# Kernel tuning notes

Measured on AMD Instinct MI355X. Metric: run time of the kernel, lower is better.

The kernel has to match this reference:

```python
import jax, jax.numpy as jnp
import numpy as np

B, S, D, H = 2, 2048, 1024, 16
DK = D // H


def setup_inputs() -> dict:
    key = jax.random.key(0)
    ks = jax.random.split(key, 8)
    Q = jax.random.normal(ks[0], (B, S, D), dtype=jnp.float32)
    K = jax.random.normal(ks[1], (B, S, D), dtype=jnp.float32)
    V = jax.random.normal(ks[2], (B, S, D), dtype=jnp.float32)
    # causal mask (1 = keep), broadcastable to [B, H, S, S]
    mask = jnp.tril(jnp.ones((S, S), dtype=bool))[None, None, :, :]
    # xavier_uniform for [D, D]: bound = sqrt(6 / (D + D))
    bound = float(np.sqrt(6.0 / (D + D)))
    def xavier(k):
        return jax.random.uniform(k, (D, D), jnp.float32, -bound, bound)
    Wq, Wk, Wv, Wo = xavier(ks[3]), xavier(ks[4]), xavier(ks[5]), xavier(ks[6])
    bq = jnp.zeros((D,), jnp.float32)
    bk = jnp.zeros((D,), jnp.float32)
    bv = jnp.zeros((D,), jnp.float32)
    bo = jnp.zeros((D,), jnp.float32)
    return {"Q": Q, "K": K, "V": V, "mask": mask,
            "Wq": Wq, "bq": bq, "Wk": Wk, "bk": bk,
            "Wv": Wv, "bv": bv, "Wo": Wo, "bo": bo}


def _split_heads(x):
    # [B, S, D] -> [B, H, S, DK]
    b, s, _ = x.shape
    return x.reshape(b, s, H, DK).transpose(0, 2, 1, 3)


def reference(Q, K, V, mask, Wq, bq, Wk, bk, Wv, bv, Wo, bo):
    # linear projections (torch Linear: x @ W.T + b)
    q = _split_heads(Q @ Wq.T + bq)  # [B, H, S, DK]
    k = _split_heads(K @ Wk.T + bk)
    v = _split_heads(V @ Wv.T + bv)
    scale = 1.0 / jnp.sqrt(jnp.asarray(DK, q.dtype))
    scores = jnp.einsum('bhqd,bhkd->bhqk', q, k) * scale  # [B, H, S, S]
    scores = jnp.where(mask, scores, jnp.asarray(-1e9, scores.dtype))
    attn = jax.nn.softmax(scores, axis=-1)
    ctx = jnp.einsum('bhqk,bhkd->bhqd', attn, v)  # [B, H, S, DK]
    ctx = ctx.transpose(0, 2, 1, 3).reshape(Q.shape[0], Q.shape[1], D)
    out = ctx @ Wo.T + bo  # dropout is identity in eval mode
    return out, attn
```

## Files before the change

### kernel.cpp

```cpp
#include <hip/hip_runtime.h>
#include <hip/hip_bf16.h>

#define B_  2
#define S_  2048
#define D_  1024
#define H_  16
#define DK_ 64
#define M_  (B_*S_)
#define NT_ (S_/64)
#define NE_ (B_*S_*D_)
#define NW_ (D_*D_)

typedef __attribute__((ext_vector_type(8))) short short8;
typedef __attribute__((ext_vector_type(4))) float f32x4;

static __device__ __forceinline__ unsigned short f2bf(float f) {
    union { float f; unsigned u; } v; v.f = f;
    unsigned r = (v.u + 0x7fffu + ((v.u >> 16) & 1u)) >> 16;
    return (unsigned short)r;
}

static __device__ __forceinline__ void gload16(const void* g, void* l) {
    __builtin_amdgcn_global_load_lds((const __attribute__((address_space(1))) void*)g,
                                     (__attribute__((address_space(3))) void*)l, 16, 0, 0);
}

__global__ __launch_bounds__(256) void conv7(const float* __restrict__ q,  const float* __restrict__ k,
                                             const float* __restrict__ v,  const float* __restrict__ wq,
                                             const float* __restrict__ wk, const float* __restrict__ wv,
                                             const float* __restrict__ wo, unsigned short* __restrict__ ws)
{
    const float* src[7] = {q, k, v, wq, wk, wv, wo};
    const int    n4[7]  = {NE_/4, NE_/4, NE_/4, NW_/4, NW_/4, NW_/4, NW_/4};
    size_t off = 0;
    #pragma unroll
    for (int seg = 0; seg < 7; ++seg) {
        unsigned short* dst = ws + off;
        for (int i = blockIdx.x*256 + threadIdx.x; i < n4[seg]; i += gridDim.x*256) {
            float4 x = ((const float4*)src[seg])[i];
            union { unsigned short u[4]; unsigned long long ll; } cv;
            cv.u[0]=f2bf(x.x); cv.u[1]=f2bf(x.y); cv.u[2]=f2bf(x.z); cv.u[3]=f2bf(x.w);
            ((unsigned long long*)dst)[i] = cv.ll;
        }
        off += (size_t)n4[seg]*4;
    }
}

__global__ __launch_bounds__(256) void gemm_bt(const unsigned short* __restrict__ A0,
                                               const unsigned short* __restrict__ W0,
                                               const float* __restrict__ b0,
                                               const float* __restrict__ b1,
                                               const float* __restrict__ b2,
                                               void* __restrict__ outv, int out_mode)
{
    __shared__ unsigned short as2[2][128][64];
    __shared__ unsigned short bs2[2][64][64];

    const int tid  = threadIdx.x;
    const int wave = tid >> 6;
    const int lane = tid & 63;
    const int lq   = lane & 15, quad = lane >> 4;
    const int z    = blockIdx.z;
    const int m0   = blockIdx.y * 128, n0 = blockIdx.x * 64;
    const int wm   = (wave >> 1) * 64, wn = (wave & 1) * 32;

    const unsigned short* A  = A0 + (size_t)z * NE_;
    const unsigned short* Bt = W0 + (size_t)z * NW_;
    const float* bias = (z == 0) ? b0 : (z == 1 ? b1 : b2);

    f32x4 acc[4][2] = {};

    auto STAGE = [&](int k0, int buf) {
        #pragma unroll
        for (int i = 0; i < 4; ++i) {
            const int p = tid + i*256, row = p >> 3, c = (p & 7) ^ (row & 7);
            gload16(A + (size_t)(m0+row)*D_ + k0 + c*8,
                    (char*)&as2[buf][0][0] + (size_t)(wave*64 + i*256)*16);
        }
        #pragma unroll
        for (int i = 0; i < 2; ++i) {
            const int p = tid + i*256, row = p >> 3, c = (p & 7) ^ (row & 7);
            gload16(Bt + (size_t)(n0+row)*D_ + k0 + c*8,
                    (char*)&bs2[buf][0][0] + (size_t)(wave*64 + i*256)*16);
        }
    };

    STAGE(0, 0);
    __syncthreads();
    int cur = 0;
    for (int k0 = 0; k0 < D_; k0 += 64) {
        if (k0 + 64 < D_) STAGE(k0 + 64, cur ^ 1);
        #pragma unroll
        for (int kk = 0; kk < 2; ++kk) {
            short8 a[4], b[2];
            #pragma unroll
            for (int i = 0; i < 4; ++i) {
                const int row = wm + i*16 + lq;
                a[i] = *(const short8*)((const char*)&as2[cur][0][0] + row*128 + (((kk*4+quad) ^ (row&7))*16));
            }
            #pragma unroll
            for (int j = 0; j < 2; ++j) {
                const int row = wn + j*16 + lq;
                b[j] = *(const short8*)((const char*)&bs2[cur][0][0] + row*128 + (((kk*4+quad) ^ (row&7))*16));
            }
            #pragma unroll
            for (int i = 0; i < 4; ++i)
                #pragma unroll
                for (int j = 0; j < 2; ++j)
                    acc[i][j] = __builtin_amdgcn_mfma_f32_16x16x32_bf16(a[i], b[j], acc[i][j], 0, 0, 0);
        }
        __syncthreads();
        cur ^= 1;
    }

    float bcol[2];
    #pragma unroll
    for (int j = 0; j < 2; ++j) bcol[j] = bias[n0 + wn + j*16 + lq];

    if (out_mode == 0) {
        float* out = (float*)outv;
        #pragma unroll
        for (int i = 0; i < 4; ++i)
            #pragma unroll
            for (int j = 0; j < 2; ++j) {
                const int col = n0 + wn + j*16 + lq;
                #pragma unroll
                for (int r = 0; r < 4; ++r) {
                    const int m = m0 + wm + i*16 + quad*4 + r;
                    out[(size_t)m*D_ + col] = acc[i][j][r] + bcol[j];
                }
            }
    } else {
        unsigned short* out = (unsigned short*)outv + (size_t)z * NE_;
        #pragma unroll
        for (int i = 0; i < 4; ++i)
            #pragma unroll
            for (int j = 0; j < 2; ++j) {
                const int col = n0 + wn + j*16 + lq;
                const int h = col >> 6, dk = col & 63;
                #pragma unroll
                for (int r = 0; r < 4; ++r) {
                    const int m  = m0 + wm + i*16 + quad*4 + r;
                    const int bb = m >> 11, s = m & (S_-1);
                    out[(((size_t)(bb*H_ + h))*S_ + s)*DK_ + dk] = f2bf(acc[i][j][r] + bcol[j]);
                }
            }
    }
}

__global__ __launch_bounds__(256) void transpose_v(const unsigned short* __restrict__ vp,
                                                   unsigned short* __restrict__ vt)
{
    __shared__ unsigned short ts[64][72];
    const int tid = threadIdx.x;
    const int s0  = blockIdx.x * 64;
    const size_t bh = (size_t)blockIdx.z * H_ + blockIdx.y;
    const unsigned short* src = vp + (bh * S_ + s0) * DK_;
    #pragma unroll
    for (int i = 0; i < 2; ++i) {
        int idx = tid + i*256;
        *(short8*)&ts[idx >> 3][(idx & 7)*8] = *(const short8*)(src + idx*8);
    }
    __syncthreads();
    unsigned short* dst = vt + bh * DK_ * S_;
    #pragma unroll
    for (int i = 0; i < 2; ++i) {
        int idx = tid + i*256;
        int dk = idx >> 3, c = idx & 7;
        union { unsigned short u[8]; short8 v; } pk;
        #pragma unroll
        for (int j = 0; j < 8; ++j) pk.u[j] = ts[c*8 + j][dk];
        *(short8*)(dst + (size_t)dk*S_ + s0 + c*8) = pk.v;
    }
}

__global__ __launch_bounds__(512) void attn_mfma(const unsigned short* __restrict__ q,
                                                 const unsigned short* __restrict__ k,
                                                 const unsigned short* __restrict__ vt,
                                                 float* __restrict__ attn,
                                                 unsigned short* __restrict__ ctx)
{
    __shared__ unsigned short qs_es[9216];
    __shared__ unsigned short ks2[2][64][64];
    __shared__ unsigned short vts2[2][64][64];

    const int tid  = threadIdx.x;
    const int wave = tid >> 6, lane = tid & 63;
    const int lq   = lane & 15, quad = lane >> 4;
    const int ts   = wave >> 2;
    const int wr0  = (wave & 3) * 16;

    const int g = blockIdx.x;
    const int xcd = g & 7, i5 = g >> 3;
    const int x = i5 >> 2;
    const int bhid = xcd + 8*(i5 & 3);
    const int h = bhid & (H_-1), b = bhid >> 4;

    const int itA = x, itB = NT_-1 - x;
    const int itM = ts ? itB : itA;
    const size_t bh = (size_t)(b*H_ + h);
    const unsigned short* kb  = k  + bh*S_*DK_;
    const unsigned short* vtb = vt + bh*(size_t)DK_*S_;
    const unsigned short* qbA = q + (bh*S_ + (size_t)itA*64) * DK_;
    const unsigned short* qbB = q + (bh*S_ + (size_t)itB*64) * DK_;
    float* attn_bM = attn + bh*(size_t)S_*S_ + (size_t)itM*64*S_;

    {
        const int row = tid >> 3, c = (tid & 7) ^ (row & 7);
        gload16(qbA + (size_t)row*DK_ + c*8, (char*)qs_es + tid*16);
        gload16(qbB + (size_t)row*DK_ + c*8, (char*)qs_es + 8192 + tid*16);
        gload16(kb  + (size_t)row*DK_ + c*8, (char*)&ks2[0][0][0] + tid*16);
    }
    __syncthreads();

    short8 aT0, aT1;
    {
        const int row = wr0 + lq;
        const char* qrow = (const char*)qs_es + ts*8192 + row*128;
        aT0 = *(const short8*)(qrow + ((quad     ^ (row & 7)) * 16));
        aT1 = *(const short8*)(qrow + (((4+quad) ^ (row & 7)) * 16));
    }
    const int rg0 = itM*64 + wr0 + quad*4;

    float rs[4] = {0.f, 0.f, 0.f, 0.f};
    int cur = 0;
    for (int jt = 0; jt <= itB; ++jt) {
        if (jt < itB) {
            const int row = tid >> 3, c = (tid & 7) ^ (row & 7);
            gload16(kb + ((size_t)(jt+1)*64 + row)*DK_ + c*8,
                    (char*)&ks2[cur^1][0][0] + tid*16);
        }
        if (jt <= itM) {
            f32x4 sa[4];
            __builtin_amdgcn_s_setprio(1);
            #pragma unroll
            for (int j = 0; j < 4; ++j) {
                const int krow = j*16 + lq;
                const char* kp8 = (const char*)&ks2[cur][0][0] + krow*128;
                const short8 b0 = *(const short8*)(kp8 + ((quad     ^ (krow&7)) * 16));
                const short8 b1 = *(const short8*)(kp8 + (((4+quad) ^ (krow&7)) * 16));
                f32x4 s = {};
                s = __builtin_amdgcn_mfma_f32_16x16x32_bf16(aT0, b0, s, 0, 0, 0);
                s = __builtin_amdgcn_mfma_f32_16x16x32_bf16(aT1, b1, s, 0, 0, 0);
                sa[j] = s;
            }
            __builtin_amdgcn_s_setprio(0);
            #pragma unroll
            for (int j = 0; j < 4; ++j) {
                const int cg = jt*64 + j*16 + lq;
                #pragma unroll
                for (int r = 0; r < 4; ++r)
                    if (cg <= rg0 + r) rs[r] += __expf(sa[j][r]*0.125f);
            }
        }
        __syncthreads();
        cur ^= 1;
    }

    {
        const int row = tid >> 3, c = (tid & 7) ^ (row & 7);
        gload16(kb  + (size_t)row*DK_ + c*8, (char*)&ks2[0][0][0]  + tid*16);
        gload16(vtb + (size_t)row*S_  + c*8, (char*)&vts2[0][0][0] + tid*16);
    }
    #pragma unroll
    for (int m = 1; m < 16; m <<= 1)
        #pragma unroll
        for (int r = 0; r < 4; ++r) rs[r] += __shfl_xor(rs[r], m, 64);
    float inv[4];
    #pragma unroll
    for (int r = 0; r < 4; ++r) inv[r] = 1.0f / rs[r];
    __syncthreads();

    unsigned short* es = qs_es;
    f32x4 cacc[4] = {};
    cur = 0;
    for (int jt = 0; jt <= itB; ++jt) {
        if (jt < itB) {
            const int row = tid >> 3, c = (tid & 7) ^ (row & 7);
            gload16(kb  + ((size_t)(jt+1)*64 + row)*DK_ + c*8,
                    (char*)&ks2[cur^1][0][0]  + tid*16);
            gload16(vtb + (size_t)row*S_ + (jt+1)*64 + c*8,
                    (char*)&vts2[cur^1][0][0] + tid*16);
        }
        if (jt <= itM) {
            f32x4 sa[4];
            __builtin_amdgcn_s_setprio(1);
            #pragma unroll
            for (int j = 0; j < 4; ++j) {
                const int krow = j*16 + lq;
                const char* kp8 = (const char*)&ks2[cur][0][0] + krow*128;
                const short8 b0 = *(const short8*)(kp8 + ((quad     ^ (krow&7)) * 16));
                const short8 b1 = *(const short8*)(kp8 + (((4+quad) ^ (krow&7)) * 16));
                f32x4 s = {};
                s = __builtin_amdgcn_mfma_f32_16x16x32_bf16(aT0, b0, s, 0, 0, 0);
                s = __builtin_amdgcn_mfma_f32_16x16x32_bf16(aT1, b1, s, 0, 0, 0);
                sa[j] = s;
            }
            __builtin_amdgcn_s_setprio(0);
            #pragma unroll
            for (int j = 0; j < 4; ++j) {
                const int cg = jt*64 + j*16 + lq;
                #pragma unroll
                for (int r = 0; r < 4; ++r) {
                    const float e = (cg <= rg0 + r) ? __expf(sa[j][r]*0.125f)*inv[r] : 0.f;
                    attn_bM[(size_t)(wr0 + quad*4 + r)*S_ + cg] = e;
                    es[wave*1152 + (quad*4 + r)*72 + j*16 + lq] = f2bf(e);
                }
            }
            const short8 p0 = *(const short8*)&es[wave*1152 + lq*72 + quad*8];
            const short8 p1 = *(const short8*)&es[wave*1152 + lq*72 + 32 + quad*8];
            __builtin_amdgcn_s_setprio(1);
            #pragma unroll
            for (int j = 0; j < 4; ++j) {
                const int vrow = j*16 + lq;
                const char* vp8 = (const char*)&vts2[cur][0][0] + vrow*128;
                cacc[j] = __builtin_amdgcn_mfma_f32_16x16x32_bf16(
                    p0, *(const short8*)(vp8 + ((quad     ^ (vrow&7)) * 16)), cacc[j], 0, 0, 0);
                cacc[j] = __builtin_amdgcn_mfma_f32_16x16x32_bf16(
                    p1, *(const short8*)(vp8 + (((4+quad) ^ (vrow&7)) * 16)), cacc[j], 0, 0, 0);
            }
            __builtin_amdgcn_s_setprio(0);
        }
        __syncthreads();
        cur ^= 1;
    }

    #pragma unroll
    for (int j = 0; j < 4; ++j) {
        const int dk = j*16 + lq;
        #pragma unroll
        for (int r = 0; r < 4; ++r) {
            const int srow = itM*64 + wr0 + quad*4 + r;
            ctx[((size_t)b*S_ + srow)*D_ + h*DK_ + dk] = f2bf(cacc[j][r]);
        }
    }

    const float4 z4 = make_float4(0.f, 0.f, 0.f, 0.f);
    {
        const int t = tid & 255;
        const int zc0 = (itM + 1) * 64;
        if (zc0 < S_) {
            float* rowp = attn_bM + (size_t)(t >> 2)*S_;
            for (int c = zc0 + (t & 3)*4; c < S_; c += 16) *(float4*)&rowp[c] = z4;
        }
    }
}

extern "C" void kernel_launch(void* const* d_in, const int* in_sizes, int n_in,
                              void* d_out, int out_size, void* d_ws, size_t ws_size,
                              hipStream_t stream)
{
    const float* Q  = (const float*)d_in[0];
    const float* K  = (const float*)d_in[1];
    const float* V  = (const float*)d_in[2];
    const float* Wq = (const float*)d_in[4];
    const float* bq = (const float*)d_in[5];
    const float* Wk = (const float*)d_in[6];
    const float* bk = (const float*)d_in[7];
    const float* Wv = (const float*)d_in[8];
    const float* bv = (const float*)d_in[9];
    const float* Wo = (const float*)d_in[10];
    const float* bo = (const float*)d_in[11];

    float* out  = (float*)d_out;
    float* attn = out + (size_t)B_*S_*D_;

    unsigned short* ws = (unsigned short*)d_ws;
    const size_t R  = (size_t)NE_;
    const size_t W1 = (size_t)NW_;
    unsigned short* Qb  = ws;
    unsigned short* Wqb = ws + 3*R;
    unsigned short* Wob = Wqb + 3*W1;
    unsigned short* qp  = Wob + W1;
    unsigned short* kp  = qp + R;
    unsigned short* vp  = qp + 2*R;
    unsigned short* vtw = qp + 3*R;
    unsigned short* ctx = vtw + R;

    conv7<<<2048, 256, 0, stream>>>(Q, K, V, Wq, Wk, Wv, Wo, ws);

    gemm_bt<<<dim3(D_/64, M_/128, 3), 256, 0, stream>>>(Qb, Wqb, bq, bk, bv, qp, 1);
    transpose_v<<<dim3(S_/64, H_, B_), 256, 0, stream>>>(vp, vtw);
    attn_mfma<<<(NT_/2)*H_*B_, 512, 0, stream>>>(qp, kp, vtw, attn, ctx);
    gemm_bt<<<dim3(D_/64, M_/128, 1), 256, 0, stream>>>(ctx, Wob, bo, bo, bo, out, 0);
}
```

Baseline: 816.7 us.

## Enlarge GEMM tiles to 128x128 with XCD-aware block mapping, single-buffer LDS

The projection GEMM tile grows from 128x64 to 128x128, so each wave computes a 64x64 sub-tile with more MFMA per LDS load. Blocks are remapped from a 1D grid so that each XCD handles a contiguous band of M rows, aiming for better L2 reuse of A. The double-buffered LDS prefetch is replaced by a single buffer with two barriers per K step. This exposes load latency and halves the number of blocks. Separately, the attention kernel's zero-fill of the masked upper region moves earlier, before the PV phase.

```diff
diff --git a/kernel.cpp b/kernel.cpp
--- a/kernel.cpp
+++ b/kernel.cpp
@@ -53,76 +53,79 @@
                                                const float* __restrict__ b2,
                                                void* __restrict__ outv, int out_mode)
 {
-    __shared__ unsigned short as2[2][128][64];
-    __shared__ unsigned short bs2[2][64][64];
+    __shared__ unsigned short as_[128][64];
+    __shared__ unsigned short bs_[128][64];
 
     const int tid  = threadIdx.x;
     const int wave = tid >> 6;
     const int lane = tid & 63;
     const int lq   = lane & 15, quad = lane >> 4;
-    const int z    = blockIdx.z;
-    const int m0   = blockIdx.y * 128, n0 = blockIdx.x * 64;
-    const int wm   = (wave >> 1) * 64, wn = (wave & 1) * 32;
+
+    const int g     = blockIdx.x;
+    const int xcd   = g & 7;
+    const int local = g >> 3;
+    const int m_loc = local & 3;
+    const int rest  = local >> 2;
+    const int n_t   = rest & 7;
+    const int z     = rest >> 3;
+
+    const int m0 = (xcd*4 + m_loc) * 128;
+    const int n0 = n_t * 128;
+    const int wm = (wave >> 1) * 64, wn = (wave & 1) * 64;
 
     const unsigned short* A  = A0 + (size_t)z * NE_;
     const unsigned short* Bt = W0 + (size_t)z * NW_;
     const float* bias = (z == 0) ? b0 : (z == 1 ? b1 : b2);
 
-    f32x4 acc[4][2] = {};
-
-    auto STAGE = [&](int k0, int buf) {
+    f32x4 acc[4][4] = {};
+
+    for (int k0 = 0; k0 < D_; k0 += 64) {
+        __syncthreads();
         #pragma unroll
         for (int i = 0; i < 4; ++i) {
             const int p = tid + i*256, row = p >> 3, c = (p & 7) ^ (row & 7);
             gload16(A + (size_t)(m0+row)*D_ + k0 + c*8,
-                    (char*)&as2[buf][0][0] + (size_t)(wave*64 + i*256)*16);
-        }
-        #pragma unroll
-        for (int i = 0; i < 2; ++i) {
+                    (char*)as_ + (size_t)(wave*64 + i*256)*16);
+        }
+        #pragma unroll
+        for (int i = 0; i < 4; ++i) {
             const int p = tid + i*256, row = p >> 3, c = (p & 7) ^ (row & 7);
             gload16(Bt + (size_t)(n0+row)*D_ + k0 + c*8,
-                    (char*)&bs2[buf][0][0] + (size_t)(wave*64 + i*256)*16);
-        }
-    };
-
-    STAGE(0, 0);
-    __syncthreads();
-    int cur = 0;
-    for (int k0 = 0; k0 < D_; k0 += 64) {
-        if (k0 + 64 < D_) STAGE(k0 + 64, cur ^ 1);
+                    (char*)bs_ + (size_t)(wave*64 + i*256)*16);
+        }
+        __syncthreads();
+
         #pragma unroll
         for (int kk = 0; kk < 2; ++kk) {
-            short8 a[4], b[2];
+            short8 a[4], b[4];
             #pragma unroll
             for (int i = 0; i < 4; ++i) {
                 const int row = wm + i*16 + lq;
-                a[i] = *(const short8*)((const char*)&as2[cur][0][0] + row*128 + (((kk*4+quad) ^ (row&7))*16));
-            }
-            #pragma unroll
-            for (int j = 0; j < 2; ++j) {
+                a[i] = *(const short8*)((const char*)as_ + row*128 + (((kk*4+quad) ^ (row&7))*16));
+            }
+            #pragma unroll
+            for (int j = 0; j < 4; ++j) {
                 const int row = wn + j*16 + lq;
-                b[j] = *(const short8*)((const char*)&bs2[cur][0][0] + row*128 + (((kk*4+quad) ^ (row&7))*16));
+                b[j] = *(const short8*)((const char*)bs_ + row*128 + (((kk*4+quad) ^ (row&7))*16));
             }
             #pragma unroll
             for (int i = 0; i < 4; ++i)
                 #pragma unroll
-                for (int j = 0; j < 2; ++j)
+                for (int j = 0; j < 4; ++j)
                     acc[i][j] = __builtin_amdgcn_mfma_f32_16x16x32_bf16(a[i], b[j], acc[i][j], 0, 0, 0);
         }
-        __syncthreads();
-        cur ^= 1;
-    }
-
-    float bcol[2];
-    #pragma unroll
-    for (int j = 0; j < 2; ++j) bcol[j] = bias[n0 + wn + j*16 + lq];
+    }
+
+    float bcol[4];
+    #pragma unroll
+    for (int j = 0; j < 4; ++j) bcol[j] = bias[n0 + wn + j*16 + lq];
 
     if (out_mode == 0) {
         float* out = (float*)outv;
         #pragma unroll
         for (int i = 0; i < 4; ++i)
             #pragma unroll
-            for (int j = 0; j < 2; ++j) {
+            for (int j = 0; j < 4; ++j) {
                 const int col = n0 + wn + j*16 + lq;
                 #pragma unroll
                 for (int r = 0; r < 4; ++r) {
@@ -135,7 +138,7 @@
         #pragma unroll
         for (int i = 0; i < 4; ++i)
             #pragma unroll
-            for (int j = 0; j < 2; ++j) {
+            for (int j = 0; j < 4; ++j) {
                 const int col = n0 + wn + j*16 + lq;
                 const int h = col >> 6, dk = col & 63;
                 #pragma unroll
@@ -255,6 +258,16 @@
         }
         __syncthreads();
         cur ^= 1;
+    }
+
+    {
+        const float4 z4 = make_float4(0.f, 0.f, 0.f, 0.f);
+        const int t = tid & 255;
+        const int zc0 = (itM + 1) * 64;
+        if (zc0 < S_) {
+            float* rowp = attn_bM + (size_t)(t >> 2)*S_;
+            for (int c = zc0 + (t & 3)*4; c < S_; c += 16) *(float4*)&rowp[c] = z4;
+        }
     }
 
     {
@@ -332,16 +345,6 @@
         for (int r = 0; r < 4; ++r) {
             const int srow = itM*64 + wr0 + quad*4 + r;
             ctx[((size_t)b*S_ + srow)*D_ + h*DK_ + dk] = f2bf(cacc[j][r]);
-        }
-    }
-
-    const float4 z4 = make_float4(0.f, 0.f, 0.f, 0.f);
-    {
-        const int t = tid & 255;
-        const int zc0 = (itM + 1) * 64;
-        if (zc0 < S_) {
-            float* rowp = attn_bM + (size_t)(t >> 2)*S_;
-            for (int c = zc0 + (t & 3)*4; c < S_; c += 16) *(float4*)&rowp[c] = z4;
         }
     }
 }
@@ -379,8 +382,8 @@
 
     conv7<<<2048, 256, 0, stream>>>(Q, K, V, Wq, Wk, Wv, Wo, ws);
 
-    gemm_bt<<<dim3(D_/64, M_/128, 3), 256, 0, stream>>>(Qb, Wqb, bq, bk, bv, qp, 1);
+    gemm_bt<<<768, 256, 0, stream>>>(Qb, Wqb, bq, bk, bv, qp, 1);
     transpose_v<<<dim3(S_/64, H_, B_), 256, 0, stream>>>(vp, vtw);
     attn_mfma<<<(NT_/2)*H_*B_, 512, 0, stream>>>(qp, kp, vtw, attn, ctx);
-    gemm_bt<<<dim3(D_/64, M_/128, 1), 256, 0, stream>>>(ctx, Wob, bo, bo, bo, out, 0);
-}
+    gemm_bt<<<256, 256, 0, stream>>>(ctx, Wob, bo, bo, bo, out, 0);
+}
```

Result: no change. 816.6 us (-0.0%).
